# Kernel optimization log

Hardware: AMD Instinct MI355X
Metric: run time of the kernel (lower is better)

Reference implementation:

```python
import jax, jax.numpy as jnp
import numpy as np

N_NODES = 50000
N_EDGES = 400000
NUM_GRAPHS = 64
D = 128
NUM_ACTIONS = 40


def setup_inputs() -> dict:
    key = jax.random.key(0)
    ks = jax.random.split(key, 20)
    s = 1.0 / np.sqrt(D)
    inp = {
        'inputs': jax.random.normal(ks[0], (N_NODES, D), jnp.float32),
        'src': jax.random.randint(ks[1], (N_EDGES,), 0, N_NODES, jnp.int32),
        'dst': jax.random.randint(ks[2], (N_EDGES,), 0, N_NODES, jnp.int32),
        'graph_ids': jnp.sort(jax.random.randint(ks[3], (N_NODES,), 0, NUM_GRAPHS, jnp.int32)),
        'init_feats': jax.random.normal(ks[4], (N_NODES, D), jnp.float32),
        'init_graph_ids': jnp.sort(jax.random.randint(ks[5], (N_NODES,), 0, NUM_GRAPHS, jnp.int32)),
        'lead_feats': jax.random.normal(ks[6], (N_NODES, D), jnp.float32),
        'lead_graph_ids': jnp.sort(jax.random.randint(ks[7], (N_NODES,), 0, NUM_GRAPHS, jnp.int32)),
        'W1': jax.random.normal(ks[8], (D, D), jnp.float32) * s,
        'b1': jnp.zeros((D,), jnp.float32),
        'W2': jax.random.normal(ks[9], (D, D), jnp.float32) * s,
        'b2': jnp.zeros((D,), jnp.float32),
        'W3': jax.random.normal(ks[10], (D, D), jnp.float32) * s,
        'b3': jnp.zeros((D,), jnp.float32),
        'fc1_W': jax.random.normal(ks[11], (D, D), jnp.float32) * s,
        'fc1_b': jnp.zeros((D,), jnp.float32),
        'fc2_W': jax.random.normal(ks[12], (D, NUM_ACTIONS), jnp.float32) * s,
        'fc2_b': jnp.zeros((NUM_ACTIONS,), jnp.float32),
    }
    return inp


def _pool(feats, gids):
    # SumPooling over a batched graph -> [B, D]
    return jax.ops.segment_sum(feats, gids, num_segments=NUM_GRAPHS)


def _ggin_layer(h, src, dst, graph_ids, ctx_per_graph, W, b):
    # neighbor sum aggregation (message passing over edge list)
    agg = jax.ops.segment_sum(h[src], dst, num_segments=N_NODES)  # [N, D]
    h_global = _pool(h, graph_ids)                                # [B, D]
    ctx = (h_global + ctx_per_graph)[graph_ids]                   # broadcast per-graph context to nodes
    return (h + agg + ctx) @ W + b


def reference(inputs, src, dst, graph_ids, init_feats, init_graph_ids,
              lead_feats, lead_graph_ids, W1, b1, W2, b2, W3, b3,
              fc1_W, fc1_b, fc2_W, fc2_b):
    h_initial = _pool(init_feats, init_graph_ids)   # [B, D]
    h_lead = _pool(lead_feats, lead_graph_ids)      # [B, D]
    ctx = h_initial + h_lead

    h = jax.nn.relu(_ggin_layer(inputs, src, dst, graph_ids, ctx, W1, b1))
    h = jax.nn.relu(_ggin_layer(h, src, dst, graph_ids, ctx, W2, b2))
    h = jax.nn.relu(_ggin_layer(h, src, dst, graph_ids, ctx, W3, b3))

    h_global = _pool(h, graph_ids)                  # [B, D]
    h_fc = jax.nn.relu(h_global @ fc1_W + fc1_b)
    return h_fc @ fc2_W + fc2_b                     # [B, num_actions]
```

## Files before the change

kernel.cpp:

```cpp
#include <hip/hip_runtime.h>

#define D 128
#define NGRAPH 64
#define NACT 40
#define BM 64
#define LDS_STRIDE 68
#define SCAN_TPB 256
#define SCAN_EPT 8
#define SCAN_CHUNK (SCAN_TPB * SCAN_EPT)
#define GNODES 8

__global__ void pool_kernel(const float* __restrict__ feats, const int* __restrict__ gids,
                            float* __restrict__ out, int n_nodes, int chunk) {
    int t = threadIdx.x;
    int start = blockIdx.x * chunk;
    int end = start + chunk;
    if (end > n_nodes) end = n_nodes;
    if (start >= end) return;
    int cur = gids[start];
    float acc = 0.f;
    int r = start;
    while (r < end) {
        if (r + 3 < end) {
            int g0 = gids[r], g3 = gids[r + 3];
            if (g0 == cur && g3 == cur) {
                float v0 = feats[(size_t)r * D + t];
                float v1 = feats[(size_t)(r + 1) * D + t];
                float v2 = feats[(size_t)(r + 2) * D + t];
                float v3 = feats[(size_t)(r + 3) * D + t];
                acc += (v0 + v1) + (v2 + v3);
                r += 4;
                continue;
            }
        }
        int g = gids[r];
        if (g != cur) {
            atomicAdd(&out[cur * D + t], acc);
            acc = 0.f;
            cur = g;
        }
        acc += feats[(size_t)r * D + t];
        ++r;
    }
    atomicAdd(&out[cur * D + t], acc);
}

__global__ void ctxw_kernel(const float* __restrict__ hg, const float* __restrict__ ctx,
                            const float* __restrict__ W, const float* __restrict__ b,
                            float* __restrict__ out) {
    __shared__ float row[D];
    int g = blockIdx.x, t = threadIdx.x;
    row[t] = hg[g * D + t] + ctx[g * D + t];
    __syncthreads();
    float acc = b[t];
#pragma unroll 4
    for (int k = 0; k < D; ++k) acc = fmaf(row[k], W[k * D + t], acc);
    out[g * D + t] = acc;
}

__global__ __launch_bounds__(256) void mm_kernel(const float* __restrict__ H,
                                                 const float* __restrict__ W,
                                                 float* __restrict__ X, int n_rows) {
    __shared__ float hT[D * LDS_STRIDE];
    int t = threadIdx.x;
    int r0 = blockIdx.x * BM;
    int tcol = t & 31;
    int trow = t >> 5;

#pragma unroll
    for (int i = 0; i < 8; ++i) {
        int idx = t + i * 256;
        int r = idx & 63;
        int kq = idx >> 6;
        int gr = r0 + r;
        float4 v = make_float4(0.f, 0.f, 0.f, 0.f);
        if (gr < n_rows) v = *(const float4*)(H + (size_t)gr * D + kq * 4);
        int k0 = kq * 4;
        hT[(k0 + 0) * LDS_STRIDE + r] = v.x;
        hT[(k0 + 1) * LDS_STRIDE + r] = v.y;
        hT[(k0 + 2) * LDS_STRIDE + r] = v.z;
        hT[(k0 + 3) * LDS_STRIDE + r] = v.w;
    }
    __syncthreads();

    float acc[8][4];
#pragma unroll
    for (int i = 0; i < 8; ++i)
#pragma unroll
        for (int j = 0; j < 4; ++j) acc[i][j] = 0.f;

#pragma unroll 4
    for (int k = 0; k < D; ++k) {
        float4 b = *(const float4*)(W + k * D + tcol * 4);
        float a[8];
        *(float4*)&a[0] = *(const float4*)&hT[k * LDS_STRIDE + trow * 8];
        *(float4*)&a[4] = *(const float4*)&hT[k * LDS_STRIDE + trow * 8 + 4];
#pragma unroll
        for (int i = 0; i < 8; ++i) {
            acc[i][0] = fmaf(a[i], b.x, acc[i][0]);
            acc[i][1] = fmaf(a[i], b.y, acc[i][1]);
            acc[i][2] = fmaf(a[i], b.z, acc[i][2]);
            acc[i][3] = fmaf(a[i], b.w, acc[i][3]);
        }
    }

#pragma unroll
    for (int i = 0; i < 8; ++i) {
        int r = r0 + trow * 8 + i;
        if (r < n_rows) {
            float4 o = make_float4(acc[i][0], acc[i][1], acc[i][2], acc[i][3]);
            *(float4*)(X + (size_t)r * D + tcol * 4) = o;
        }
    }
}

__global__ void hist_kernel(const int* __restrict__ dst, int* __restrict__ counts, int n_edges) {
    int stride = gridDim.x * blockDim.x;
    for (int e = blockIdx.x * blockDim.x + threadIdx.x; e < n_edges; e += stride)
        atomicAdd(&counts[dst[e]], 1);
}

__global__ void scanA_kernel(const int* __restrict__ counts, int* __restrict__ rowptr,
                             int* __restrict__ blocksums, int n) {
    __shared__ int smem[SCAN_TPB];
    int b = blockIdx.x, t = threadIdx.x;
    int i0 = b * SCAN_CHUNK + t * SCAN_EPT;
    int e[SCAN_EPT];
#pragma unroll
    for (int j = 0; j < SCAN_EPT; ++j) {
        int i = i0 + j;
        e[j] = (i < n) ? counts[i] : 0;
    }
#pragma unroll
    for (int j = 1; j < SCAN_EPT; ++j) e[j] += e[j - 1];
    smem[t] = e[SCAN_EPT - 1];
    __syncthreads();
    for (int off = 1; off < SCAN_TPB; off <<= 1) {
        int u = (t >= off) ? smem[t - off] : 0;
        __syncthreads();
        smem[t] += u;
        __syncthreads();
    }
    int excl = t ? smem[t - 1] : 0;
#pragma unroll
    for (int j = 0; j < SCAN_EPT; ++j) {
        int i = i0 + j;
        if (i < n) rowptr[i + 1] = excl + e[j];
    }
    if (t == SCAN_TPB - 1) blocksums[b] = smem[t];
    if (b == 0 && t == 0) rowptr[0] = 0;
}

__global__ void scanB_kernel(int* __restrict__ blocksums, int nb) {
    if (threadIdx.x == 0 && blockIdx.x == 0) {
        int acc = 0;
        for (int i = 0; i < nb; ++i) {
            int v = blocksums[i];
            blocksums[i] = acc;
            acc += v;
        }
    }
}

__global__ void scanC_kernel(int* __restrict__ rowptr, int* __restrict__ cursor,
                             const int* __restrict__ blocksums, int n) {
    int b = blockIdx.x, t = threadIdx.x;
    int off = blocksums[b];
    int i0 = b * SCAN_CHUNK + t * SCAN_EPT;
#pragma unroll
    for (int j = 0; j < SCAN_EPT; ++j) {
        int i = i0 + j;
        if (i < n) {
            int v = rowptr[i + 1] + off;
            rowptr[i + 1] = v;
            if (i + 1 < n) cursor[i + 1] = v;
        }
    }
    if (b == 0 && t == 0) cursor[0] = 0;
}

__global__ void fill_kernel(const int* __restrict__ src, const int* __restrict__ dst,
                            int* __restrict__ cursor, int* __restrict__ srcs, int n_edges) {
    int stride = gridDim.x * blockDim.x;
    for (int e = blockIdx.x * blockDim.x + threadIdx.x; e < n_edges; e += stride) {
        int pos = atomicAdd(&cursor[dst[e]], 1);
        srcs[pos] = src[e];
    }
}

__global__ __launch_bounds__(256) void gather_kernel(const float4* __restrict__ X4,
                              const int* __restrict__ rowptr, const int* __restrict__ srcs,
                              const int* __restrict__ gids, const float4* __restrict__ ctxgW4,
                              float4* __restrict__ H4, int n_nodes) {
    int n = blockIdx.x * GNODES + (threadIdx.x >> 5);
    if (n >= n_nodes) return;
    int q = threadIdx.x & 31;
    int beg = rowptr[n], end = rowptr[n + 1];
    float4 a = X4[(size_t)n * 32 + q];
    float4 c = ctxgW4[(size_t)gids[n] * 32 + q];
    float4 acc = make_float4(a.x + c.x, a.y + c.y, a.z + c.z, a.w + c.w);
    int e = beg;
    for (; e + 4 <= end; e += 4) {
        int s0 = srcs[e + 0], s1 = srcs[e + 1], s2 = srcs[e + 2], s3 = srcs[e + 3];
        float4 v0 = X4[(size_t)s0 * 32 + q];
        float4 v1 = X4[(size_t)s1 * 32 + q];
        float4 v2 = X4[(size_t)s2 * 32 + q];
        float4 v3 = X4[(size_t)s3 * 32 + q];
        acc.x += (v0.x + v1.x) + (v2.x + v3.x);
        acc.y += (v0.y + v1.y) + (v2.y + v3.y);
        acc.z += (v0.z + v1.z) + (v2.z + v3.z);
        acc.w += (v0.w + v1.w) + (v2.w + v3.w);
    }
    for (; e < end; ++e) {
        float4 v = X4[(size_t)srcs[e] * 32 + q];
        acc.x += v.x; acc.y += v.y; acc.z += v.z; acc.w += v.w;
    }
    acc.x = fmaxf(acc.x, 0.f); acc.y = fmaxf(acc.y, 0.f);
    acc.z = fmaxf(acc.z, 0.f); acc.w = fmaxf(acc.w, 0.f);
    H4[(size_t)n * 32 + q] = acc;
}

__global__ void head_kernel(const float* __restrict__ hg,
                            const float* __restrict__ fc1W, const float* __restrict__ fc1b,
                            const float* __restrict__ fc2W, const float* __restrict__ fc2b,
                            float* __restrict__ out) {
    __shared__ float row[D];
    __shared__ float hfc[D];
    int g = blockIdx.x, t = threadIdx.x;
    row[t] = hg[g * D + t];
    __syncthreads();
    float acc = fc1b[t];
#pragma unroll 4
    for (int k = 0; k < D; ++k) acc = fmaf(row[k], fc1W[k * D + t], acc);
    hfc[t] = fmaxf(acc, 0.f);
    __syncthreads();
    if (t < NACT) {
        float o = fc2b[t];
#pragma unroll 4
        for (int k = 0; k < D; ++k) o = fmaf(hfc[k], fc2W[k * NACT + t], o);
        out[g * NACT + t] = o;
    }
}

extern "C" void kernel_launch(void* const* d_in, const int* in_sizes, int n_in,
                              void* d_out, int out_size, void* d_ws, size_t ws_size,
                              hipStream_t stream) {
    const float* inputs     = (const float*)d_in[0];
    const int*   src        = (const int*)d_in[1];
    const int*   dst        = (const int*)d_in[2];
    const int*   graph_ids  = (const int*)d_in[3];
    const float* init_feats = (const float*)d_in[4];
    const int*   init_gids  = (const int*)d_in[5];
    const float* lead_feats = (const float*)d_in[6];
    const int*   lead_gids  = (const int*)d_in[7];
    const float* Wmat[3] = { (const float*)d_in[8], (const float*)d_in[10], (const float*)d_in[12] };
    const float* bvec[3] = { (const float*)d_in[9], (const float*)d_in[11], (const float*)d_in[13] };
    const float* fc1W = (const float*)d_in[14];
    const float* fc1b = (const float*)d_in[15];
    const float* fc2W = (const float*)d_in[16];
    const float* fc2b = (const float*)d_in[17];
    float* out = (float*)d_out;

    const int n_nodes = in_sizes[0] / D;
    const int n_edges = in_sizes[1];

    float* ws    = (float*)d_ws;
    float* ctx   = ws;
    float* hg    = ctx + NGRAPH * D;
    float* ctxgW = hg + NGRAPH * D;
    float* X     = ctxgW + NGRAPH * D;
    float* Ha    = X + (size_t)n_nodes * D;
    int*   counts = (int*)(Ha + (size_t)n_nodes * D);
    int*   rowptr = counts + n_nodes;
    int*   srcs   = rowptr + n_nodes + 1;
    int*   blocksums = srcs + n_edges;

    const int POOL_CHUNK = 64;
    const int pool_blocks = (n_nodes + POOL_CHUNK - 1) / POOL_CHUNK;
    const int mm_blocks = (n_nodes + BM - 1) / BM;
    const int scan_blocks = (n_nodes + SCAN_CHUNK - 1) / SCAN_CHUNK;
    const int gather_blocks = (n_nodes + GNODES - 1) / GNODES;

    hipMemsetAsync(counts, 0, n_nodes * sizeof(int), stream);
    hist_kernel<<<1024, 256, 0, stream>>>(dst, counts, n_edges);
    scanA_kernel<<<scan_blocks, SCAN_TPB, 0, stream>>>(counts, rowptr, blocksums, n_nodes);
    scanB_kernel<<<1, 64, 0, stream>>>(blocksums, scan_blocks);
    scanC_kernel<<<scan_blocks, SCAN_TPB, 0, stream>>>(rowptr, counts, blocksums, n_nodes);
    fill_kernel<<<1024, 256, 0, stream>>>(src, dst, counts, srcs, n_edges);

    hipMemsetAsync(ctx, 0, NGRAPH * D * sizeof(float), stream);
    pool_kernel<<<pool_blocks, D, 0, stream>>>(init_feats, init_gids, ctx, n_nodes, POOL_CHUNK);
    pool_kernel<<<pool_blocks, D, 0, stream>>>(lead_feats, lead_gids, ctx, n_nodes, POOL_CHUNK);

    const float* Hcur = inputs;
    for (int layer = 0; layer < 3; ++layer) {
        hipMemsetAsync(hg, 0, NGRAPH * D * sizeof(float), stream);
        pool_kernel<<<pool_blocks, D, 0, stream>>>(Hcur, graph_ids, hg, n_nodes, POOL_CHUNK);
        ctxw_kernel<<<NGRAPH, D, 0, stream>>>(hg, ctx, Wmat[layer], bvec[layer], ctxgW);
        mm_kernel<<<mm_blocks, 256, 0, stream>>>(Hcur, Wmat[layer], X, n_nodes);
        gather_kernel<<<gather_blocks, 256, 0, stream>>>((const float4*)X, rowptr, srcs,
                                                         graph_ids, (const float4*)ctxgW,
                                                         (float4*)Ha, n_nodes);
        Hcur = Ha;
    }

    hipMemsetAsync(hg, 0, NGRAPH * D * sizeof(float), stream);
    pool_kernel<<<pool_blocks, D, 0, stream>>>(Hcur, graph_ids, hg, n_nodes, POOL_CHUNK);
    head_kernel<<<NGRAPH, D, 0, stream>>>(hg, fc1W, fc1b, fc2W, fc2b, out);
}
```

Baseline: 514.3 us.

## Store activations in bf16, use MFMA matmul, fuse pools and memsets

Node activations and the transformed features are now stored in bf16, and the per-layer matmul runs on bf16 MFMA instructions with pre-transposed bf16 weights. The gather and pooling kernels read bf16, which halves the memory traffic of the bandwidth-bound edge gather. The three initial pools become one launch, the memsets are merged into one, and the serial scanB kernel is folded into scanC. The cost is reduced precision in the intermediate activations, plus extra conversion kernels for the inputs and weights.

```diff
diff --git a/kernel.cpp b/kernel.cpp
--- a/kernel.cpp
+++ b/kernel.cpp
@@ -3,43 +3,82 @@
 #define D 128
 #define NGRAPH 64
 #define NACT 40
-#define BM 64
-#define LDS_STRIDE 68
 #define SCAN_TPB 256
 #define SCAN_EPT 8
-#define SCAN_CHUNK (SCAN_TPB * SCAN_EPT)
+#define SCAN_CHUNK 2048
 #define GNODES 8
-
-__global__ void pool_kernel(const float* __restrict__ feats, const int* __restrict__ gids,
-                            float* __restrict__ out, int n_nodes, int chunk) {
+#define POOL_CHUNK 64
+
+typedef __attribute__((ext_vector_type(8))) short bf16x8;
+typedef __attribute__((ext_vector_type(4))) float f32x4;
+typedef __attribute__((ext_vector_type(8))) unsigned short us8;
+
+__device__ inline unsigned short f2b(float f) {
+    unsigned u = __float_as_uint(f);
+    return (unsigned short)((u + 0x7FFFu + ((u >> 16) & 1u)) >> 16);
+}
+__device__ inline float b2f(unsigned short h) {
+    return __uint_as_float(((unsigned)h) << 16);
+}
+
+__global__ void pool3_kernel(const float* __restrict__ f0, const int* __restrict__ g0, float* o0,
+                             const float* __restrict__ f1, const int* __restrict__ g1, float* o1,
+                             const float* __restrict__ f2, const int* __restrict__ g2, float* o2,
+                             int n_nodes) {
+    const float* feats; const int* gids; float* out;
+    if (blockIdx.y == 0)      { feats = f0; gids = g0; out = o0; }
+    else if (blockIdx.y == 1) { feats = f1; gids = g1; out = o1; }
+    else                      { feats = f2; gids = g2; out = o2; }
     int t = threadIdx.x;
-    int start = blockIdx.x * chunk;
-    int end = start + chunk;
+    int start = blockIdx.x * POOL_CHUNK;
+    int end = start + POOL_CHUNK;
     if (end > n_nodes) end = n_nodes;
     if (start >= end) return;
     int cur = gids[start];
     float acc = 0.f;
     int r = start;
     while (r < end) {
-        if (r + 3 < end) {
-            int g0 = gids[r], g3 = gids[r + 3];
-            if (g0 == cur && g3 == cur) {
-                float v0 = feats[(size_t)r * D + t];
-                float v1 = feats[(size_t)(r + 1) * D + t];
-                float v2 = feats[(size_t)(r + 2) * D + t];
-                float v3 = feats[(size_t)(r + 3) * D + t];
-                acc += (v0 + v1) + (v2 + v3);
-                r += 4;
-                continue;
-            }
+        if (r + 3 < end && gids[r] == cur && gids[r + 3] == cur) {
+            float v0 = feats[(size_t)r * D + t];
+            float v1 = feats[(size_t)(r + 1) * D + t];
+            float v2 = feats[(size_t)(r + 2) * D + t];
+            float v3 = feats[(size_t)(r + 3) * D + t];
+            acc += (v0 + v1) + (v2 + v3);
+            r += 4;
+            continue;
         }
         int g = gids[r];
-        if (g != cur) {
-            atomicAdd(&out[cur * D + t], acc);
-            acc = 0.f;
-            cur = g;
-        }
+        if (g != cur) { atomicAdd(&out[cur * D + t], acc); acc = 0.f; cur = g; }
         acc += feats[(size_t)r * D + t];
+        ++r;
+    }
+    atomicAdd(&out[cur * D + t], acc);
+}
+
+__global__ void pool_b16_kernel(const unsigned short* __restrict__ feats,
+                                const int* __restrict__ gids, float* __restrict__ out,
+                                int n_nodes) {
+    int t = threadIdx.x;
+    int start = blockIdx.x * POOL_CHUNK;
+    int end = start + POOL_CHUNK;
+    if (end > n_nodes) end = n_nodes;
+    if (start >= end) return;
+    int cur = gids[start];
+    float acc = 0.f;
+    int r = start;
+    while (r < end) {
+        if (r + 3 < end && gids[r] == cur && gids[r + 3] == cur) {
+            float v0 = b2f(feats[(size_t)r * D + t]);
+            float v1 = b2f(feats[(size_t)(r + 1) * D + t]);
+            float v2 = b2f(feats[(size_t)(r + 2) * D + t]);
+            float v3 = b2f(feats[(size_t)(r + 3) * D + t]);
+            acc += (v0 + v1) + (v2 + v3);
+            r += 4;
+            continue;
+        }
+        int g = gids[r];
+        if (g != cur) { atomicAdd(&out[cur * D + t], acc); acc = 0.f; cur = g; }
+        acc += b2f(feats[(size_t)r * D + t]);
         ++r;
     }
     atomicAdd(&out[cur * D + t], acc);
@@ -58,58 +97,69 @@
     out[g * D + t] = acc;
 }
 
-__global__ __launch_bounds__(256) void mm_kernel(const float* __restrict__ H,
-                                                 const float* __restrict__ W,
-                                                 float* __restrict__ X, int n_rows) {
-    __shared__ float hT[D * LDS_STRIDE];
+__global__ void conv_kernel(const float4* __restrict__ in4, ushort4* __restrict__ out4, int n4) {
+    int stride = gridDim.x * blockDim.x;
+    for (int i = blockIdx.x * blockDim.x + threadIdx.x; i < n4; i += stride) {
+        float4 v = in4[i];
+        ushort4 o;
+        o.x = f2b(v.x); o.y = f2b(v.y); o.z = f2b(v.z); o.w = f2b(v.w);
+        out4[i] = o;
+    }
+}
+
+__global__ void wconv_kernel(const float* __restrict__ W0, const float* __restrict__ W1,
+                             const float* __restrict__ W2, unsigned short* __restrict__ WTb) {
+    const float* W = blockIdx.y == 0 ? W0 : (blockIdx.y == 1 ? W1 : W2);
+    unsigned short* WT = WTb + blockIdx.y * (D * D);
+    int idx = blockIdx.x * 256 + threadIdx.x;
+    int n = idx >> 7, k = idx & 127;
+    WT[n * D + k] = f2b(W[k * D + n]);
+}
+
+__global__ __launch_bounds__(256) void mm_mfma(const unsigned short* __restrict__ Hb,
+                                               const unsigned short* __restrict__ WT,
+                                               unsigned short* __restrict__ X, int n_rows) {
+    __shared__ unsigned short aT[64 * 136];
+    __shared__ unsigned short bT[128 * 136];
     int t = threadIdx.x;
-    int r0 = blockIdx.x * BM;
-    int tcol = t & 31;
-    int trow = t >> 5;
-
-#pragma unroll
-    for (int i = 0; i < 8; ++i) {
-        int idx = t + i * 256;
-        int r = idx & 63;
-        int kq = idx >> 6;
-        int gr = r0 + r;
-        float4 v = make_float4(0.f, 0.f, 0.f, 0.f);
-        if (gr < n_rows) v = *(const float4*)(H + (size_t)gr * D + kq * 4);
-        int k0 = kq * 4;
-        hT[(k0 + 0) * LDS_STRIDE + r] = v.x;
-        hT[(k0 + 1) * LDS_STRIDE + r] = v.y;
-        hT[(k0 + 2) * LDS_STRIDE + r] = v.z;
-        hT[(k0 + 3) * LDS_STRIDE + r] = v.w;
-    }
-    __syncthreads();
-
-    float acc[8][4];
-#pragma unroll
-    for (int i = 0; i < 8; ++i)
-#pragma unroll
-        for (int j = 0; j < 4; ++j) acc[i][j] = 0.f;
-
-#pragma unroll 4
-    for (int k = 0; k < D; ++k) {
-        float4 b = *(const float4*)(W + k * D + tcol * 4);
-        float a[8];
-        *(float4*)&a[0] = *(const float4*)&hT[k * LDS_STRIDE + trow * 8];
-        *(float4*)&a[4] = *(const float4*)&hT[k * LDS_STRIDE + trow * 8 + 4];
-#pragma unroll
-        for (int i = 0; i < 8; ++i) {
-            acc[i][0] = fmaf(a[i], b.x, acc[i][0]);
-            acc[i][1] = fmaf(a[i], b.y, acc[i][1]);
-            acc[i][2] = fmaf(a[i], b.z, acc[i][2]);
-            acc[i][3] = fmaf(a[i], b.w, acc[i][3]);
-        }
-    }
-
-#pragma unroll
-    for (int i = 0; i < 8; ++i) {
-        int r = r0 + trow * 8 + i;
-        if (r < n_rows) {
-            float4 o = make_float4(acc[i][0], acc[i][1], acc[i][2], acc[i][3]);
-            *(float4*)(X + (size_t)r * D + tcol * 4) = o;
+    int r0 = blockIdx.x * 64;
+
+    for (int i = t; i < 1024; i += 256) {
+        int r = i >> 4, kq = i & 15;
+        us8 v = {0, 0, 0, 0, 0, 0, 0, 0};
+        if (r0 + r < n_rows) v = *(const us8*)(Hb + (size_t)(r0 + r) * D + kq * 8);
+        *(us8*)&aT[r * 136 + kq * 8] = v;
+    }
+    for (int i = t; i < 2048; i += 256) {
+        int n = i >> 4, kq = i & 15;
+        *(us8*)&bT[n * 136 + kq * 8] = *(const us8*)(WT + n * D + kq * 8);
+    }
+    __syncthreads();
+
+    int lane = t & 63;
+    int rbase = (t >> 6) * 16;
+    int arow = lane & 15, kgrp = lane >> 4;
+    f32x4 acc[8];
+#pragma unroll
+    for (int i = 0; i < 8; ++i) acc[i] = (f32x4){0.f, 0.f, 0.f, 0.f};
+
+#pragma unroll
+    for (int kc = 0; kc < 4; ++kc) {
+        bf16x8 a = *(bf16x8*)&aT[(rbase + arow) * 136 + kc * 32 + kgrp * 8];
+#pragma unroll
+        for (int nt = 0; nt < 8; ++nt) {
+            bf16x8 b = *(bf16x8*)&bT[(nt * 16 + arow) * 136 + kc * 32 + kgrp * 8];
+            acc[nt] = __builtin_amdgcn_mfma_f32_16x16x32_bf16(a, b, acc[nt], 0, 0, 0);
+        }
+    }
+
+    int rr = rbase + kgrp * 4;
+#pragma unroll
+    for (int nt = 0; nt < 8; ++nt) {
+#pragma unroll
+        for (int j = 0; j < 4; ++j) {
+            int r = r0 + rr + j;
+            if (r < n_rows) X[(size_t)r * D + nt * 16 + arow] = f2b(acc[nt][j]);
         }
     }
 }
@@ -151,21 +201,17 @@
     if (b == 0 && t == 0) rowptr[0] = 0;
 }
 
-__global__ void scanB_kernel(int* __restrict__ blocksums, int nb) {
-    if (threadIdx.x == 0 && blockIdx.x == 0) {
-        int acc = 0;
-        for (int i = 0; i < nb; ++i) {
-            int v = blocksums[i];
-            blocksums[i] = acc;
-            acc += v;
-        }
-    }
-}
-
 __global__ void scanC_kernel(int* __restrict__ rowptr, int* __restrict__ cursor,
                              const int* __restrict__ blocksums, int n) {
+    __shared__ int off_s;
     int b = blockIdx.x, t = threadIdx.x;
-    int off = blocksums[b];
+    if (t == 0) {
+        int a = 0;
+        for (int i = 0; i < b; ++i) a += blocksums[i];
+        off_s = a;
+    }
+    __syncthreads();
+    int off = off_s;
     int i0 = b * SCAN_CHUNK + t * SCAN_EPT;
 #pragma unroll
     for (int j = 0; j < SCAN_EPT; ++j) {
@@ -188,36 +234,38 @@
     }
 }
 
-__global__ __launch_bounds__(256) void gather_kernel(const float4* __restrict__ X4,
-                              const int* __restrict__ rowptr, const int* __restrict__ srcs,
-                              const int* __restrict__ gids, const float4* __restrict__ ctxgW4,
-                              float4* __restrict__ H4, int n_nodes) {
+__global__ __launch_bounds__(256) void gather_kernel(const unsigned short* __restrict__ Xb,
+        const int* __restrict__ rowptr, const int* __restrict__ srcs,
+        const int* __restrict__ gids, const float4* __restrict__ ctxgW4,
+        unsigned short* __restrict__ Hb, int n_nodes) {
     int n = blockIdx.x * GNODES + (threadIdx.x >> 5);
     if (n >= n_nodes) return;
     int q = threadIdx.x & 31;
     int beg = rowptr[n], end = rowptr[n + 1];
-    float4 a = X4[(size_t)n * 32 + q];
+    ushort4 a = *(const ushort4*)(Xb + (size_t)n * D + q * 4);
     float4 c = ctxgW4[(size_t)gids[n] * 32 + q];
-    float4 acc = make_float4(a.x + c.x, a.y + c.y, a.z + c.z, a.w + c.w);
+    float ax = b2f(a.x) + c.x, ay = b2f(a.y) + c.y;
+    float az = b2f(a.z) + c.z, aw = b2f(a.w) + c.w;
     int e = beg;
     for (; e + 4 <= end; e += 4) {
-        int s0 = srcs[e + 0], s1 = srcs[e + 1], s2 = srcs[e + 2], s3 = srcs[e + 3];
-        float4 v0 = X4[(size_t)s0 * 32 + q];
-        float4 v1 = X4[(size_t)s1 * 32 + q];
-        float4 v2 = X4[(size_t)s2 * 32 + q];
-        float4 v3 = X4[(size_t)s3 * 32 + q];
-        acc.x += (v0.x + v1.x) + (v2.x + v3.x);
-        acc.y += (v0.y + v1.y) + (v2.y + v3.y);
-        acc.z += (v0.z + v1.z) + (v2.z + v3.z);
-        acc.w += (v0.w + v1.w) + (v2.w + v3.w);
+        int s0 = srcs[e], s1 = srcs[e + 1], s2 = srcs[e + 2], s3 = srcs[e + 3];
+        ushort4 v0 = *(const ushort4*)(Xb + (size_t)s0 * D + q * 4);
+        ushort4 v1 = *(const ushort4*)(Xb + (size_t)s1 * D + q * 4);
+        ushort4 v2 = *(const ushort4*)(Xb + (size_t)s2 * D + q * 4);
+        ushort4 v3 = *(const ushort4*)(Xb + (size_t)s3 * D + q * 4);
+        ax += (b2f(v0.x) + b2f(v1.x)) + (b2f(v2.x) + b2f(v3.x));
+        ay += (b2f(v0.y) + b2f(v1.y)) + (b2f(v2.y) + b2f(v3.y));
+        az += (b2f(v0.z) + b2f(v1.z)) + (b2f(v2.z) + b2f(v3.z));
+        aw += (b2f(v0.w) + b2f(v1.w)) + (b2f(v2.w) + b2f(v3.w));
     }
     for (; e < end; ++e) {
-        float4 v = X4[(size_t)srcs[e] * 32 + q];
-        acc.x += v.x; acc.y += v.y; acc.z += v.z; acc.w += v.w;
-    }
-    acc.x = fmaxf(acc.x, 0.f); acc.y = fmaxf(acc.y, 0.f);
-    acc.z = fmaxf(acc.z, 0.f); acc.w = fmaxf(acc.w, 0.f);
-    H4[(size_t)n * 32 + q] = acc;
+        ushort4 v = *(const ushort4*)(Xb + (size_t)srcs[e] * D + q * 4);
+        ax += b2f(v.x); ay += b2f(v.y); az += b2f(v.z); aw += b2f(v.w);
+    }
+    ushort4 o;
+    o.x = f2b(fmaxf(ax, 0.f)); o.y = f2b(fmaxf(ay, 0.f));
+    o.z = f2b(fmaxf(az, 0.f)); o.w = f2b(fmaxf(aw, 0.f));
+    *(ushort4*)(Hb + (size_t)n * D + q * 4) = o;
 }
 
 __global__ void head_kernel(const float* __restrict__ hg,
@@ -264,47 +312,49 @@
     const int n_nodes = in_sizes[0] / D;
     const int n_edges = in_sizes[1];
 
-    float* ws    = (float*)d_ws;
-    float* ctx   = ws;
-    float* hg    = ctx + NGRAPH * D;
-    float* ctxgW = hg + NGRAPH * D;
-    float* X     = ctxgW + NGRAPH * D;
-    float* Ha    = X + (size_t)n_nodes * D;
-    int*   counts = (int*)(Ha + (size_t)n_nodes * D);
-    int*   rowptr = counts + n_nodes;
-    int*   srcs   = rowptr + n_nodes + 1;
-    int*   blocksums = srcs + n_edges;
-
-    const int POOL_CHUNK = 64;
+    unsigned char* p = (unsigned char*)d_ws;
+    float* ctx    = (float*)p;                          p += NGRAPH * D * sizeof(float);
+    float* hg     = (float*)p;                          p += 4 * NGRAPH * D * sizeof(float);
+    int*   counts = (int*)p;                            p += (size_t)n_nodes * sizeof(int);
+    size_t zero_bytes = (size_t)(p - (unsigned char*)d_ws);
+    int*   rowptr = (int*)p;                            p += ((size_t)n_nodes + 1) * sizeof(int);
+    int*   blocksums = (int*)p;                         p += 64 * sizeof(int);
+    float* ctxgW  = (float*)p;                          p += NGRAPH * D * sizeof(float);
+    int*   srcs   = (int*)p;                            p += (size_t)n_edges * sizeof(int);
+    p = (unsigned char*)(((uintptr_t)p + 15) & ~(uintptr_t)15);
+    unsigned short* Hbf = (unsigned short*)p;           p += (size_t)n_nodes * D * sizeof(short);
+    unsigned short* Xbf = (unsigned short*)p;           p += (size_t)n_nodes * D * sizeof(short);
+    unsigned short* WTb = (unsigned short*)p;           p += 3 * D * D * sizeof(short);
+
     const int pool_blocks = (n_nodes + POOL_CHUNK - 1) / POOL_CHUNK;
-    const int mm_blocks = (n_nodes + BM - 1) / BM;
+    const int mm_blocks = (n_nodes + 63) / 64;
     const int scan_blocks = (n_nodes + SCAN_CHUNK - 1) / SCAN_CHUNK;
     const int gather_blocks = (n_nodes + GNODES - 1) / GNODES;
-
-    hipMemsetAsync(counts, 0, n_nodes * sizeof(int), stream);
+    const int n4 = n_nodes * D / 4;
+
+    hipMemsetAsync(ctx, 0, zero_bytes, stream);
+
     hist_kernel<<<1024, 256, 0, stream>>>(dst, counts, n_edges);
     scanA_kernel<<<scan_blocks, SCAN_TPB, 0, stream>>>(counts, rowptr, blocksums, n_nodes);
-    scanB_kernel<<<1, 64, 0, stream>>>(blocksums, scan_blocks);
     scanC_kernel<<<scan_blocks, SCAN_TPB, 0, stream>>>(rowptr, counts, blocksums, n_nodes);
     fill_kernel<<<1024, 256, 0, stream>>>(src, dst, counts, srcs, n_edges);
 
-    hipMemsetAsync(ctx, 0, NGRAPH * D * sizeof(float), stream);
-    pool_kernel<<<pool_blocks, D, 0, stream>>>(init_feats, init_gids, ctx, n_nodes, POOL_CHUNK);
-    pool_kernel<<<pool_blocks, D, 0, stream>>>(lead_feats, lead_gids, ctx, n_nodes, POOL_CHUNK);
-
-    const float* Hcur = inputs;
+    conv_kernel<<<2048, 256, 0, stream>>>((const float4*)inputs, (ushort4*)Hbf, n4);
+    wconv_kernel<<<dim3(64, 3), 256, 0, stream>>>(Wmat[0], Wmat[1], Wmat[2], WTb);
+
+    pool3_kernel<<<dim3(pool_blocks, 3), D, 0, stream>>>(
+        init_feats, init_gids, ctx, lead_feats, lead_gids, ctx,
+        inputs, graph_ids, hg, n_nodes);
+
     for (int layer = 0; layer < 3; ++layer) {
-        hipMemsetAsync(hg, 0, NGRAPH * D * sizeof(float), stream);
-        pool_kernel<<<pool_blocks, D, 0, stream>>>(Hcur, graph_ids, hg, n_nodes, POOL_CHUNK);
-        ctxw_kernel<<<NGRAPH, D, 0, stream>>>(hg, ctx, Wmat[layer], bvec[layer], ctxgW);
-        mm_kernel<<<mm_blocks, 256, 0, stream>>>(Hcur, Wmat[layer], X, n_nodes);
-        gather_kernel<<<gather_blocks, 256, 0, stream>>>((const float4*)X, rowptr, srcs,
-                                                         graph_ids, (const float4*)ctxgW,
-                                                         (float4*)Ha, n_nodes);
-        Hcur = Ha;
-    }
-
-    hipMemsetAsync(hg, 0, NGRAPH * D * sizeof(float), stream);
-    pool_kernel<<<pool_blocks, D, 0, stream>>>(Hcur, graph_ids, hg, n_nodes, POOL_CHUNK);
-    head_kernel<<<NGRAPH, D, 0, stream>>>(hg, fc1W, fc1b, fc2W, fc2b, out);
-}
+        float* hgL = hg + layer * NGRAPH * D;
+        ctxw_kernel<<<NGRAPH, D, 0, stream>>>(hgL, ctx, Wmat[layer], bvec[layer], ctxgW);
+        mm_mfma<<<mm_blocks, 256, 0, stream>>>(Hbf, WTb + layer * D * D, Xbf, n_nodes);
+        gather_kernel<<<gather_blocks, 256, 0, stream>>>(Xbf, rowptr, srcs, graph_ids,
+                                                         (const float4*)ctxgW, Hbf, n_nodes);
+        pool_b16_kernel<<<pool_blocks, D, 0, stream>>>(Hbf, graph_ids,
+                                                       hg + (layer + 1) * NGRAPH * D, n_nodes);
+    }
+
+    head_kernel<<<NGRAPH, D, 0, stream>>>(hg + 3 * NGRAPH * D, fc1W, fc1b, fc2W, fc2b, out);
+}
```

Result: faster. 416.0 us (-19.1%).
